# Kernel tuning notes

Hardware: AMD Instinct MI355X
Metric: run time of the kernel (lower is better)

## Reference

```python
import math
import jax, jax.numpy as jnp
import numpy as np

# TreeAttention (HiP-style hierarchical top-k mask) hyperparameters
K = 64          # self.k: retained keys per query
W0 = 64         # self.w: initial coarse window
SCALE_UP = 2.0
OVERSAMPLE = 1.5
NEG = -32000.0  # masked score fill used inside the pruning loop
FMIN = -1e30    # masked score fill for final softmax


def _gather_rows(m, idx):
    # m: [N, C, H], idx: [N, A, Z] -> [N, A, Z, H]
    return jnp.take_along_axis(m[:, None, :, :], idx[:, :, :, None], axis=2)


def _masked_scores(q, k, xs, xs_mask, value):
    # jax equivalent of masked_bmm_masked_indices (sampled_addmm on a CSR mask):
    # only compute q . k[xs] at the Z listed columns per query row.
    C = k.shape[1]
    kg = _gather_rows(k, jnp.minimum(xs, C - 1))          # [N, A, Z, H]
    s = jnp.einsum('nah,nazh->naz', q, kg)
    return jnp.where(xs_mask > 0.5, s, value)


def _dedup_rows(ps):
    # ps: [R, L] sorted ascending per row. Replicates torch
    # unique_consecutive(return_inverse) + per-row min-subtract + scatter:
    # compact distinct values to the front, fill the rest with -1.
    first = jnp.ones((ps.shape[0], 1), dtype=bool)
    is_new = jnp.concatenate([first, ps[:, 1:] != ps[:, :-1]], axis=1)
    ranks = jnp.cumsum(is_new, axis=1) - 1                # rank of distinct value in row
    rows = jnp.arange(ps.shape[0])[:, None]
    out = jnp.full_like(ps, -1)
    return out.at[rows, ranks].set(ps)  # duplicate ranks write identical values


def _forward_mask(q, k):
    N, T_SRC, HID = k.shape
    _, T_DST, _ = q.shape
    start = T_SRC - T_DST + 1
    tsrcs = jnp.arange(start, start + T_DST, dtype=jnp.float32)[None, :, None]  # [1,T_DST,1]
    w = W0
    ws = jnp.full((N, T_DST, 1), float(W0), dtype=jnp.float32)
    max_pixels = max(int(round(K * OVERSAMPLE)), W0)
    pixels = jnp.broadcast_to(jnp.arange(max_pixels, dtype=jnp.int32)[None, None, :],
                              (N, T_DST, max_pixels))
    pmask = jnp.broadcast_to((jnp.arange(max_pixels) < W0).astype(jnp.float32)[None, None, :],
                             (N, T_DST, max_pixels))
    MAX_SU = int(math.ceil(SCALE_UP))
    while True:  # static loop: w doubles 64 -> 4096, 7 iterations
        is_last = (w == T_SRC)
        Z = pixels.shape[-1]
        # --- topk_mask: score the current candidate pixels, keep top tks ---
        txs = jnp.round(pixels * (tsrcs / ws)).astype(jnp.int32)
        scores = _masked_scores(q, k, txs, pmask, NEG)
        mult = 1.0 if is_last else OVERSAMPLE
        tks = jnp.clip(jnp.round(ws / tsrcs * K * mult), 1.0,
                       jnp.minimum(ws - 1.0, float(Z - 1))).astype(jnp.int32)  # [N,T_DST,1]
        tks_max = int(math.ceil(min(w - 1, Z - 1, K * mult)))
        _, idx = jax.lax.top_k(scores, tks_max)
        new_pixels = jnp.take_along_axis(pixels, idx, axis=-1)
        new_pmask = (jnp.arange(tks_max)[None, None, :] < tks).astype(jnp.float32)
        pixels = jnp.pad(new_pixels, ((0, 0), (0, 0), (0, Z - tks_max)))
        pmask = jnp.pad(new_pmask, ((0, 0), (0, 0), (0, Z - tks_max)))
        # --- update per-row window, then resize pixels into the finer grid ---
        ws_new = jnp.minimum(tsrcs, ws * SCALE_UP)
        scale = ws_new / ws
        ps_start = jnp.round(pixels * scale).astype(jnp.int32)
        ps_end = jnp.round((pixels + 1) * scale).astype(jnp.int32)
        ps = jnp.broadcast_to(ps_start[..., None], (N, T_DST, Z, MAX_SU))
        counts = (ps_end - ps_start)[..., None]
        reps = jnp.arange(MAX_SU, dtype=jnp.float32)[None, None, None, :] * pmask[..., None]
        ps = ps + jnp.minimum(reps, jnp.maximum(counts - 1, 0).astype(jnp.float32)).astype(jnp.int32)
        ps = jnp.sort(ps.reshape(N * T_DST, Z * MAX_SU), axis=-1)
        ps = _dedup_rows(ps).reshape(N, T_DST, -1)
        pmask = (ps >= 0).astype(jnp.float32)
        pixels = jnp.where(ps < 0, 0, ps)
        max_z = K if is_last else int(round(K * 2))
        pixels = pixels[..., :max_z]
        pmask = pmask[..., :max_z]
        ws = ws_new
        if is_last:
            break
        w = min(T_SRC, w * SCALE_UP)
    return pixels, pmask  # CSR mask: per-query column indices + validity mask


def setup_inputs() -> dict:
    key = jax.random.key(0)
    kq, kk, kv = jax.random.split(key, 3)
    N, T_DST, T_SRC, HID = 8, 512, 4096, 64
    q = jax.random.normal(kq, (N, T_DST, HID), dtype=jnp.float32)
    k = jax.random.normal(kk, (N, T_SRC, HID), dtype=jnp.float32)
    v = jax.random.normal(kv, (N, T_SRC, HID), dtype=jnp.float32)
    return {"q": q, "k": k, "v": v}


def reference(q, k, v):
    pixels, pmask = _forward_mask(q, k)          # [N,T_DST,K] int, [N,T_DST,K] {0,1}
    kg = _gather_rows(k, pixels)                 # [N,T_DST,K,H]
    vg = _gather_rows(v, pixels)
    s = jnp.einsum('nah,nazh->naz', q, kg)
    s = jnp.where(pmask > 0.5, s, FMIN)
    p = jax.nn.softmax(s, axis=-1)
    return jnp.einsum('naz,nazh->nah', p, vg)    # [N, T_DST, HID]
```

## Files before the change

### kernel.cpp

```cpp
#include <hip/hip_runtime.h>
#include <math.h>


#define TSRC_N 4096
#define HID_N  64
#define NEGV   -32000.0f

__global__ __launch_bounds__(128)
void tree_attn_kernel(const float* __restrict__ q,
                      const float* __restrict__ k,
                      const float* __restrict__ v,
                      float* __restrict__ out)
{
    const int row  = blockIdx.x;
    const int n    = row >> 9;
    const float tsrc = (float)(3585 + (row & 511));
    const int tid  = threadIdx.x;
    const int lane = tid & 63;
    const int wid  = tid >> 6;

    __shared__ __align__(16) float q_s[HID_N];
    __shared__ int                 pix_s[128];
    __shared__ unsigned char       msk_s[128];
    __shared__ unsigned long long  key_s[128];
    __shared__ unsigned int        bm[128];
    __shared__ int                 wtot_s[2];
    __shared__ double              p_s[64];

    const float* kb = k + (size_t)n * TSRC_N * HID_N;
    const float* vb = v + (size_t)n * TSRC_N * HID_N;

    if (tid < HID_N) q_s[tid] = q[(size_t)row * HID_N + tid];
    pix_s[tid] = tid;
    msk_s[tid] = (tid < 64) ? 1 : 0;
    __syncthreads();

    float ws = 64.0f;
    int Z = 96;

    for (int it = 0; it < 7; ++it) {
        const bool  last    = (it == 6);
        const float mult    = last ? 1.0f : 1.5f;
        const int   tks_max = (it == 0) ? 63 : (last ? 64 : 96);
        const int   max_z   = last ? 64 : 128;

        unsigned long long mykey = 0;
        if (tid < Z) {
            float myscore = NEGV;
            if (msk_s[tid]) {
                const float r = tsrc / ws;
                int tx = (int)rintf((float)pix_s[tid] * r);
                tx = tx < (TSRC_N - 1) ? tx : (TSRC_N - 1);
                const float4* k4 = (const float4*)(kb + (size_t)tx * HID_N);
                const float4* q4 = (const float4*)q_s;
                double acc = 0.0;
                #pragma unroll
                for (int h4 = 0; h4 < HID_N / 4; ++h4) {
                    const float4 kv = k4[h4];
                    const float4 qv = q4[h4];
                    acc = fma((double)qv.x, (double)kv.x, acc);
                    acc = fma((double)qv.y, (double)kv.y, acc);
                    acc = fma((double)qv.z, (double)kv.z, acc);
                    acc = fma((double)qv.w, (double)kv.w, acc);
                }
                myscore = (float)acc;
            }
            const unsigned int u  = __float_as_uint(myscore);
            const unsigned int ok = u ^ ((unsigned)((int)u >> 31) | 0x80000000u);
            mykey = ((unsigned long long)ok << 7) | (unsigned)(127 - tid);
        }
        key_s[tid] = mykey;
        bm[tid] = 0u;
        __syncthreads();

        int rank = 0;
        {
            #pragma unroll 8
            for (int j = 0; j < 128; ++j)
                rank += (int)(key_s[j] > mykey);
        }

        float x = ws / tsrc;
        x *= 64.0f;
        x *= mult;
        float t = rintf(x);
        t = fmaxf(1.0f, fminf(t, fminf(ws - 1.0f, (float)(Z - 1))));
        const int tks = (int)t;

        const float ws_new = fminf(tsrc, ws * 2.0f);
        const float scale  = ws_new / ws;

        if (tid == 0) atomicOr(&bm[0], 1u);
        if (tid < Z && rank < tks_max) {
            const int p  = pix_s[tid];
            int s0 = (int)rintf((float)p * scale);
            s0 = s0 < (TSRC_N - 1) ? s0 : (TSRC_N - 1);
            atomicOr(&bm[s0 >> 5], 1u << (s0 & 31));
            if (rank < tks) {
                const int s1 = (int)rintf((float)(p + 1) * scale);
                if (s1 - s0 >= 2) {
                    const int c = s0 + 1;
                    atomicOr(&bm[c >> 5], 1u << (c & 31));
                }
            }
        }
        __syncthreads();

        const unsigned int myw = bm[tid];
        const int c = __popc(myw);
        int scan = c;
        #pragma unroll
        for (int off = 1; off < 64; off <<= 1) {
            const int o = __shfl_up(scan, off);
            if (lane >= off) scan += o;
        }
        if (lane == 63) wtot_s[wid] = scan;
        pix_s[tid] = 0;
        msk_s[tid] = 0;
        __syncthreads();
        int pref = scan - c + (wid ? wtot_s[0] : 0);

        unsigned int wv = myw;
        while (wv) {
            if (pref >= max_z) break;
            const int b = __ffs(wv) - 1;
            wv &= wv - 1u;
            pix_s[pref] = (tid << 5) + b;
            msk_s[pref] = 1;
            ++pref;
        }
        __syncthreads();

        ws = ws_new;
        Z  = max_z;
    }

    if (tid < 64) {
        double sfin = -1e30;
        if (msk_s[tid]) {
            const float4* k4 = (const float4*)(kb + (size_t)pix_s[tid] * HID_N);
            const float4* q4 = (const float4*)q_s;
            double acc = 0.0;
            #pragma unroll
            for (int h4 = 0; h4 < HID_N / 4; ++h4) {
                const float4 kv = k4[h4];
                const float4 qv = q4[h4];
                acc = fma((double)qv.x, (double)kv.x, acc);
                acc = fma((double)qv.y, (double)kv.y, acc);
                acc = fma((double)qv.z, (double)kv.z, acc);
                acc = fma((double)qv.w, (double)kv.w, acc);
            }
            sfin = acc;
        }
        double m = sfin;
        #pragma unroll
        for (int off = 32; off > 0; off >>= 1)
            m = fmax(m, __shfl_xor(m, off));
        const double e = exp(sfin - m);
        double ssum = e;
        #pragma unroll
        for (int off = 32; off > 0; off >>= 1)
            ssum += __shfl_xor(ssum, off);
        p_s[tid] = e / ssum;
    }
    __syncthreads();

    if (tid < 64) {
        double acc = 0.0;
        for (int j = 0; j < 64; ++j)
            acc = fma(p_s[j], (double)vb[(size_t)pix_s[j] * HID_N + tid], acc);
        out[(size_t)row * HID_N + tid] = (float)acc;
    }
}

extern "C" void kernel_launch(void* const* d_in, const int* in_sizes, int n_in,
                              void* d_out, int out_size, void* d_ws, size_t ws_size,
                              hipStream_t stream) {
    const float* q = (const float*)d_in[0];
    const float* k = (const float*)d_in[1];
    const float* v = (const float*)d_in[2];
    float* out = (float*)d_out;
    const int rows = in_sizes[0] / HID_N;
    tree_attn_kernel<<<rows, 128, 0, stream>>>(q, k, v, out);
}
```

Baseline: 180.0 us.

## Use single-wavefront blocks with fp32 dots and 32-bit sort keys

Each row is now handled by one 64-lane wavefront instead of 128 threads, with every lane owning two candidates. The double-precision dot products and softmax are replaced by fp32 with four partial accumulators and __expf. Ranking switches from 64-bit keys with tie-break bits to 32-bit keys read as vectors, and the cross-wave scan now happens within one wave. The intent is to remove FP64 throughput cost and cross-wave synchronisation. In exchange, dropping the index tie-break means candidates with equal scores share a rank, and fp32 accumulation can change top-k selection near ties.

```diff
diff --git a/kernel.cpp b/kernel.cpp
--- a/kernel.cpp
+++ b/kernel.cpp
@@ -6,7 +6,7 @@
 #define HID_N  64
 #define NEGV   -32000.0f
 
-__global__ __launch_bounds__(128)
+__global__ __launch_bounds__(64)
 void tree_attn_kernel(const float* __restrict__ q,
                       const float* __restrict__ k,
                       const float* __restrict__ v,
@@ -15,24 +15,40 @@
     const int row  = blockIdx.x;
     const int n    = row >> 9;
     const float tsrc = (float)(3585 + (row & 511));
-    const int tid  = threadIdx.x;
-    const int lane = tid & 63;
-    const int wid  = tid >> 6;
-
-    __shared__ __align__(16) float q_s[HID_N];
-    __shared__ int                 pix_s[128];
-    __shared__ unsigned char       msk_s[128];
-    __shared__ unsigned long long  key_s[128];
-    __shared__ unsigned int        bm[128];
-    __shared__ int                 wtot_s[2];
-    __shared__ double              p_s[64];
-
-    const float* kb = k + (size_t)n * TSRC_N * HID_N;
-    const float* vb = v + (size_t)n * TSRC_N * HID_N;
-
-    if (tid < HID_N) q_s[tid] = q[(size_t)row * HID_N + tid];
-    pix_s[tid] = tid;
-    msk_s[tid] = (tid < 64) ? 1 : 0;
+    const int lane = threadIdx.x;
+
+    __shared__ __align__(16) unsigned int key_s[128];
+    __shared__ __align__(16) unsigned int bm[128];
+    __shared__ int                        pix_s[128];
+    __shared__ unsigned char              msk_s[128];
+    __shared__ __align__(8) unsigned int  pp_s[128];
+
+    const float* qrow = q + (size_t)row * HID_N;
+    const float* kb   = k + (size_t)n * TSRC_N * HID_N;
+    const float* vb   = v + (size_t)n * TSRC_N * HID_N;
+
+    auto dot_f32 = [&](int tx) -> float {
+        const float4* k4 = (const float4*)(kb + (size_t)tx * HID_N);
+        float a0 = 0.f, a1 = 0.f, a2 = 0.f, a3 = 0.f;
+        #pragma unroll
+        for (int h4 = 0; h4 < HID_N / 4; ++h4) {
+            const float4 kv = k4[h4];
+            a0 = fmaf(kv.x, qrow[h4 * 4 + 0], a0);
+            a1 = fmaf(kv.y, qrow[h4 * 4 + 1], a1);
+            a2 = fmaf(kv.z, qrow[h4 * 4 + 2], a2);
+            a3 = fmaf(kv.w, qrow[h4 * 4 + 3], a3);
+        }
+        return (a0 + a1) + (a2 + a3);
+    };
+    auto flip32 = [](float s) -> unsigned int {
+        const unsigned int u = __float_as_uint(s);
+        return u ^ ((unsigned)((int)u >> 31) | 0x80000000u);
+    };
+
+    pix_s[lane]      = lane;
+    pix_s[lane + 64] = lane + 64;
+    msk_s[lane]      = 1;
+    msk_s[lane + 64] = 0;
     __syncthreads();
 
     float ws = 64.0f;
@@ -43,41 +59,42 @@
         const float mult    = last ? 1.0f : 1.5f;
         const int   tks_max = (it == 0) ? 63 : (last ? 64 : 96);
         const int   max_z   = last ? 64 : 128;
-
-        unsigned long long mykey = 0;
-        if (tid < Z) {
-            float myscore = NEGV;
-            if (msk_s[tid]) {
-                const float r = tsrc / ws;
-                int tx = (int)rintf((float)pix_s[tid] * r);
+        const int   e1      = lane + 64;
+
+        const float r = tsrc / ws;
+        unsigned int key0 = 0, key1 = 0;
+        {
+            float s0 = NEGV;
+            if (msk_s[lane]) {
+                int tx = (int)rintf((float)pix_s[lane] * r);
                 tx = tx < (TSRC_N - 1) ? tx : (TSRC_N - 1);
-                const float4* k4 = (const float4*)(kb + (size_t)tx * HID_N);
-                const float4* q4 = (const float4*)q_s;
-                double acc = 0.0;
-                #pragma unroll
-                for (int h4 = 0; h4 < HID_N / 4; ++h4) {
-                    const float4 kv = k4[h4];
-                    const float4 qv = q4[h4];
-                    acc = fma((double)qv.x, (double)kv.x, acc);
-                    acc = fma((double)qv.y, (double)kv.y, acc);
-                    acc = fma((double)qv.z, (double)kv.z, acc);
-                    acc = fma((double)qv.w, (double)kv.w, acc);
-                }
-                myscore = (float)acc;
-            }
-            const unsigned int u  = __float_as_uint(myscore);
-            const unsigned int ok = u ^ ((unsigned)((int)u >> 31) | 0x80000000u);
-            mykey = ((unsigned long long)ok << 7) | (unsigned)(127 - tid);
-        }
-        key_s[tid] = mykey;
-        bm[tid] = 0u;
-        __syncthreads();
-
-        int rank = 0;
-        {
-            #pragma unroll 8
-            for (int j = 0; j < 128; ++j)
-                rank += (int)(key_s[j] > mykey);
+                s0 = dot_f32(tx);
+            }
+            key0 = flip32(s0);
+        }
+        if (e1 < Z) {
+            float s1 = NEGV;
+            if (msk_s[e1]) {
+                int tx = (int)rintf((float)pix_s[e1] * r);
+                tx = tx < (TSRC_N - 1) ? tx : (TSRC_N - 1);
+                s1 = dot_f32(tx);
+            }
+            key1 = flip32(s1);
+        }
+        key_s[lane] = key0;
+        key_s[e1]   = key1;
+        bm[lane]    = 0u;
+        bm[e1]      = 0u;
+        __syncthreads();
+
+        int r0 = 0, r1 = 0;
+        #pragma unroll 8
+        for (int j = 0; j < 128; j += 4) {
+            const uint4 kk = *(const uint4*)&key_s[j];
+            r0 += (int)(kk.x > key0) + (int)(kk.y > key0)
+                + (int)(kk.z > key0) + (int)(kk.w > key0);
+            r1 += (int)(kk.x > key1) + (int)(kk.y > key1)
+                + (int)(kk.z > key1) + (int)(kk.w > key1);
         }
 
         float x = ws / tsrc;
@@ -90,42 +107,65 @@
         const float ws_new = fminf(tsrc, ws * 2.0f);
         const float scale  = ws_new / ws;
 
-        if (tid == 0) atomicOr(&bm[0], 1u);
-        if (tid < Z && rank < tks_max) {
-            const int p  = pix_s[tid];
+        if (lane == 0) atomicOr(&bm[0], 1u);
+        if (r0 < tks_max) {
+            const int p  = pix_s[lane];
             int s0 = (int)rintf((float)p * scale);
             s0 = s0 < (TSRC_N - 1) ? s0 : (TSRC_N - 1);
             atomicOr(&bm[s0 >> 5], 1u << (s0 & 31));
-            if (rank < tks) {
-                const int s1 = (int)rintf((float)(p + 1) * scale);
-                if (s1 - s0 >= 2) {
+            if (r0 < tks) {
+                const int s1i = (int)rintf((float)(p + 1) * scale);
+                if (s1i - s0 >= 2) {
                     const int c = s0 + 1;
                     atomicOr(&bm[c >> 5], 1u << (c & 31));
                 }
             }
         }
-        __syncthreads();
-
-        const unsigned int myw = bm[tid];
-        const int c = __popc(myw);
+        if (e1 < Z && r1 < tks_max) {
+            const int p  = pix_s[e1];
+            int s0 = (int)rintf((float)p * scale);
+            s0 = s0 < (TSRC_N - 1) ? s0 : (TSRC_N - 1);
+            atomicOr(&bm[s0 >> 5], 1u << (s0 & 31));
+            if (r1 < tks) {
+                const int s1i = (int)rintf((float)(p + 1) * scale);
+                if (s1i - s0 >= 2) {
+                    const int c = s0 + 1;
+                    atomicOr(&bm[c >> 5], 1u << (c & 31));
+                }
+            }
+        }
+        __syncthreads();
+
+        const uint2 w2 = *(const uint2*)&bm[2 * lane];
+        const int c = __popc(w2.x) + __popc(w2.y);
         int scan = c;
         #pragma unroll
         for (int off = 1; off < 64; off <<= 1) {
             const int o = __shfl_up(scan, off);
             if (lane >= off) scan += o;
         }
-        if (lane == 63) wtot_s[wid] = scan;
-        pix_s[tid] = 0;
-        msk_s[tid] = 0;
-        __syncthreads();
-        int pref = scan - c + (wid ? wtot_s[0] : 0);
-
-        unsigned int wv = myw;
+        int pref = scan - c;
+        pix_s[lane] = 0;  pix_s[e1] = 0;
+        msk_s[lane] = 0;  msk_s[e1] = 0;
+        __syncthreads();
+
+        unsigned int wv = w2.x;
+        int base = lane << 6;
         while (wv) {
             if (pref >= max_z) break;
             const int b = __ffs(wv) - 1;
             wv &= wv - 1u;
-            pix_s[pref] = (tid << 5) + b;
+            pix_s[pref] = base + b;
+            msk_s[pref] = 1;
+            ++pref;
+        }
+        wv = w2.y;
+        base += 32;
+        while (wv) {
+            if (pref >= max_z) break;
+            const int b = __ffs(wv) - 1;
+            wv &= wv - 1u;
+            pix_s[pref] = base + b;
             msk_s[pref] = 1;
             ++pref;
         }
@@ -135,41 +175,34 @@
         Z  = max_z;
     }
 
-    if (tid < 64) {
-        double sfin = -1e30;
-        if (msk_s[tid]) {
-            const float4* k4 = (const float4*)(kb + (size_t)pix_s[tid] * HID_N);
-            const float4* q4 = (const float4*)q_s;
-            double acc = 0.0;
-            #pragma unroll
-            for (int h4 = 0; h4 < HID_N / 4; ++h4) {
-                const float4 kv = k4[h4];
-                const float4 qv = q4[h4];
-                acc = fma((double)qv.x, (double)kv.x, acc);
-                acc = fma((double)qv.y, (double)kv.y, acc);
-                acc = fma((double)qv.z, (double)kv.z, acc);
-                acc = fma((double)qv.w, (double)kv.w, acc);
-            }
-            sfin = acc;
-        }
-        double m = sfin;
+    {
+        const int pix = pix_s[lane];
+        float sfin = -1e30f;
+        if (msk_s[lane]) sfin = dot_f32(pix);
+        float m = sfin;
         #pragma unroll
         for (int off = 32; off > 0; off >>= 1)
-            m = fmax(m, __shfl_xor(m, off));
-        const double e = exp(sfin - m);
-        double ssum = e;
+            m = fmaxf(m, __shfl_xor(m, off));
+        const float e = __expf(sfin - m);
+        float ssum = e;
         #pragma unroll
         for (int off = 32; off > 0; off >>= 1)
             ssum += __shfl_xor(ssum, off);
-        p_s[tid] = e / ssum;
+        const float p = e / ssum;
+        pp_s[2 * lane]     = __float_as_uint(p);
+        pp_s[2 * lane + 1] = (unsigned int)pix;
     }
     __syncthreads();
 
-    if (tid < 64) {
-        double acc = 0.0;
-        for (int j = 0; j < 64; ++j)
-            acc = fma(p_s[j], (double)vb[(size_t)pix_s[j] * HID_N + tid], acc);
-        out[(size_t)row * HID_N + tid] = (float)acc;
+    {
+        float acc = 0.f;
+        #pragma unroll 4
+        for (int j = 0; j < 64; ++j) {
+            const uint2 pp = *(const uint2*)&pp_s[2 * j];
+            acc = fmaf(__uint_as_float(pp.x),
+                       vb[(size_t)pp.y * HID_N + lane], acc);
+        }
+        out[(size_t)row * HID_N + lane] = acc;
     }
 }
 
@@ -181,5 +214,5 @@
     const float* v = (const float*)d_in[2];
     float* out = (float*)d_out;
     const int rows = in_sizes[0] / HID_N;
-    tree_attn_kernel<<<rows, 128, 0, stream>>>(q, k, v, out);
+    tree_attn_kernel<<<rows, 64, 0, stream>>>(q, k, v, out);
 }
```

After: 166.6 us. -7.4%, faster.
